# Performance work log

Hardware: AMD Instinct MI355X
Metric: run time of the kernel (lower is better)

## Reference

```python
import jax, jax.numpy as jnp
import numpy as np

B, S, D, L, H = 8, 1024, 512, 6, 8
HD = D // H


def setup_inputs() -> dict:
    key = jax.random.key(0)
    sc = D ** -0.5
    inp = {
        "xr": jax.random.normal(jax.random.fold_in(key, 0), (B, S, D), jnp.float32),
        "xi": jax.random.normal(jax.random.fold_in(key, 1), (B, S, D), jnp.float32),
    }
    wnames = ["Wq_r", "Wq_i", "Wk_r", "Wk_i", "Wv_r", "Wv_i", "Wo_r", "Wo_i",
              "W1_r", "W1_i", "W2_r", "W2_i"]
    for i, n in enumerate(wnames):
        inp[n] = jax.random.normal(jax.random.fold_in(key, 10 + i), (L, D, D), jnp.float32) * sc
    for n in ["bq_r", "bq_i", "bk_r", "bk_i", "bv_r", "bv_i", "bo_r", "bo_i",
              "b1_r", "b1_i", "b2_r", "b2_i"]:
        inp[n] = jnp.zeros((L, D), jnp.float32)
    g0 = 1.0 / np.sqrt(2.0)  # standard complex-LN affine init
    for n in ["ln1_grr", "ln1_gii", "ln2_grr", "ln2_gii"]:
        inp[n] = jnp.full((L, D), g0, jnp.float32)
    for n in ["ln1_gri", "ln1_br", "ln1_bi", "ln2_gri", "ln2_br", "ln2_bi"]:
        inp[n] = jnp.zeros((L, D), jnp.float32)
    return inp


def clin(xr, xi, Wr, Wi, br, bi):
    # ComplexLinear: (xr + i xi)(Wr + i Wi)^T + (br + i bi)
    yr = xr @ Wr.T - xi @ Wi.T + br
    yi = xr @ Wi.T + xi @ Wr.T + bi
    return yr, yi


def cln(xr, xi, grr, gri, gii, br, bi, eps=1e-5):
    # Complex LayerNorm: 2x2 covariance whitening over the feature dim + affine
    mr = xr.mean(-1, keepdims=True)
    mi = xi.mean(-1, keepdims=True)
    cr, ci = xr - mr, xi - mi
    Vrr = (cr * cr).mean(-1, keepdims=True) + eps
    Vii = (ci * ci).mean(-1, keepdims=True) + eps
    Vri = (cr * ci).mean(-1, keepdims=True)
    s = jnp.sqrt(Vrr * Vii - Vri * Vri)
    t = jnp.sqrt(Vrr + Vii + 2.0 * s)
    st = s * t
    Wrr = (Vii + s) / st
    Wii = (Vrr + s) / st
    Wri = -Vri / st
    hr = Wrr * cr + Wri * ci
    hi = Wri * cr + Wii * ci
    return grr * hr + gri * hi + br, gri * hr + gii * hi + bi


def reference(xr, xi,
              Wq_r, Wq_i, bq_r, bq_i, Wk_r, Wk_i, bk_r, bk_i,
              Wv_r, Wv_i, bv_r, bv_i, Wo_r, Wo_i, bo_r, bo_i,
              W1_r, W1_i, b1_r, b1_i, W2_r, W2_i, b2_r, b2_i,
              ln1_grr, ln1_gri, ln1_gii, ln1_br, ln1_bi,
              ln2_grr, ln2_gri, ln2_gii, ln2_br, ln2_bi):
    b, s, d = xr.shape
    nl = Wq_r.shape[0]
    h = H
    hd = d // h
    scale = hd ** -0.5
    for l in range(nl):
        rr, ri = xr, xi
        qr, qi = clin(xr, xi, Wq_r[l], Wq_i[l], bq_r[l], bq_i[l])
        kr, ki = clin(xr, xi, Wk_r[l], Wk_i[l], bk_r[l], bk_i[l])
        vr, vi = clin(xr, xi, Wv_r[l], Wv_i[l], bv_r[l], bv_i[l])
        split = lambda a: a.reshape(b, s, h, hd)
        qr, qi, kr, ki, vr, vi = map(split, (qr, qi, kr, ki, vr, vi))
        # sm_variante='real': softmax over Re(q k^H) = qr.kr + qi.ki
        logits = (jnp.einsum('bqhd,bkhd->bhqk', qr, kr)
                  + jnp.einsum('bqhd,bkhd->bhqk', qi, ki)) * scale
        A = jax.nn.softmax(logits, axis=-1)  # real-valued attention weights
        o_r = jnp.einsum('bhqk,bkhd->bqhd', A, vr).reshape(b, s, d)
        o_i = jnp.einsum('bhqk,bkhd->bqhd', A, vi).reshape(b, s, d)
        o_r, o_i = clin(o_r, o_i, Wo_r[l], Wo_i[l], bo_r[l], bo_i[l])
        xr, xi = o_r + rr, o_i + ri
        xr, xi = cln(xr, xi, ln1_grr[l], ln1_gri[l], ln1_gii[l], ln1_br[l], ln1_bi[l])
        rr, ri = xr, xi
        hr, hi = clin(xr, xi, W1_r[l], W1_i[l], b1_r[l], b1_i[l])
        hr, hi = jax.nn.relu(hr), jax.nn.relu(hi)  # CReLU; dropout = identity (eval)
        hr, hi = clin(hr, hi, W2_r[l], W2_i[l], b2_r[l], b2_i[l])
        xr, xi = hr + rr, hi + ri
        xr, xi = cln(xr, xi, ln2_grr[l], ln2_gri[l], ln2_gii[l], ln2_br[l], ln2_bi[l])
    return jnp.stack([xr, xi])  # [2, B, S, D] (real, imag)
```

## Files before the change

### kernel.cpp

```cpp
#include <hip/hip_runtime.h>
#include <cstddef>
#include <cstdint>

constexpr int NB   = 8;
constexpr int SEQ  = 1024;
constexpr int DIM  = 512;
constexpr int NL   = 6;
constexpr int NH   = 8;
constexpr int HDIM = 64;
constexpr int ROWS = NB * SEQ;
constexpr size_t BSD = (size_t)ROWS * DIM;
constexpr int KHAT = 1024;

typedef __attribute__((ext_vector_type(8))) short bfrag;
typedef __attribute__((ext_vector_type(4))) float f32x4;
typedef __attribute__((ext_vector_type(4))) unsigned short us4;

__device__ __forceinline__ void f4a(const float4 v, float* a) {
    a[0] = v.x; a[1] = v.y; a[2] = v.z; a[3] = v.w;
}
__device__ __forceinline__ float4 a4f(const float* a) {
    float4 v; v.x = a[0]; v.y = a[1]; v.z = a[2]; v.w = a[3]; return v;
}
__device__ __forceinline__ unsigned short f2bf(float f) {
    union { float f; uint32_t u; } x{f};
    return (unsigned short)((x.u + 0x7fffu + ((x.u >> 16) & 1u)) >> 16);
}
__device__ __forceinline__ float bf2f(unsigned short u) {
    union { uint32_t u; float f; } x;
    x.u = (uint32_t)u << 16;
    return x.f;
}
__device__ __forceinline__ void gload16(const unsigned short* g, void* l) {
    __builtin_amdgcn_global_load_lds(
        (const __attribute__((address_space(1))) void*)g,
        (__attribute__((address_space(3))) void*)l, 16, 0, 0);
}

struct PrepArgs {
    const float* Wr[6]; const float* Wi[6];
    const float* br[6]; const float* bi[6];
};

__global__ __launch_bounds__(256)
void prep_kernel(PrepArgs a, unsigned short* __restrict__ Ball,
                 float* __restrict__ biasall, int layer)
{
    const int lin = blockIdx.y;
    const int nh_ = blockIdx.x;
    const float* Wr = a.Wr[lin] + (size_t)layer * DIM * DIM;
    const float* Wi = a.Wi[lin] + (size_t)layer * DIM * DIM;

    bool real; int n0;
    if (lin < 3) { const int dh = nh_ & 127; real = dh < 64; n0 = (nh_ >> 7) * 64 + (dh & 63); }
    else         { real = nh_ < 512; n0 = nh_ & 511; }

    const int t = threadIdx.x;
    const int kk = (t * 4) & 511;
    const bool fh = t < 128;
    const float* src;
    float sgn = 1.f;
    if (fh) src = real ? Wr : Wi;
    else { if (real) { src = Wi; sgn = -1.f; } else src = Wr; }

    float v[4];
    f4a(*(const float4*)(src + (size_t)n0 * 512 + kk), v);
    us4 o;
    #pragma unroll
    for (int j = 0; j < 4; ++j) o[j] = f2bf(sgn * v[j]);
    *(us4*)(Ball + (size_t)lin * KHAT * KHAT + (size_t)nh_ * KHAT + t * 4) = o;
    if (t == 0)
        biasall[lin * KHAT + nh_] = real ? a.br[lin][layer * DIM + n0]
                                         : a.bi[lin][layer * DIM + n0];
}

__global__ __launch_bounds__(256)
void gemm_qkv(const unsigned short* __restrict__ Xh,
              const unsigned short* __restrict__ Ball,
              const float* __restrict__ biasall,
              unsigned short* __restrict__ Qh,
              unsigned short* __restrict__ Kh,
              unsigned short* __restrict__ Vth)
{
    __shared__ __align__(16) unsigned short Asm[128 * 32];
    __shared__ __align__(16) unsigned short Bsm[128 * 32];

    const int t = threadIdx.x, lane = t & 63, w = t >> 6;
    const int wm = w >> 1, wn = w & 1;
    const int c = lane & 15, g = lane >> 4;

    int bid = blockIdx.y * 24 + blockIdx.x;
    bid = (bid & 7) * 192 + (bid >> 3);
    const int nblk = bid % 24, mblk = bid / 24;
    const int n0g = nblk * 128;
    const int m0 = mblk * 128;
    const int lin = n0g >> 10;
    const int n0 = n0g & 1023;
    const unsigned short* Bh = Ball + (size_t)lin * KHAT * KHAT;
    const float* bias = biasall + lin * KHAT;

    f32x4 acc[4][4];
    #pragma unroll
    for (int i = 0; i < 4; ++i)
        #pragma unroll
        for (int j = 0; j < 4; ++j) acc[i][j] = (f32x4){0.f, 0.f, 0.f, 0.f};

    const int srow = (w << 4) + (lane >> 2);
    const int scol = (lane & 3) * 8;
    const unsigned short* gA0 = Xh + (size_t)(m0 + srow) * KHAT + scol;
    const unsigned short* gA1 = Xh + (size_t)(m0 + 64 + srow) * KHAT + scol;
    const unsigned short* gB0 = Bh + (size_t)(n0 + srow) * KHAT + scol;
    const unsigned short* gB1 = Bh + (size_t)(n0 + 64 + srow) * KHAT + scol;
    char* aBase = (char*)Asm + (w << 10);
    char* bBase = (char*)Bsm + (w << 10);

    for (int ks = 0; ks < 32; ++ks) {
        const int k0 = ks * 32;
        __syncthreads();
        gload16(gA0 + k0, aBase);
        gload16(gA1 + k0, aBase + 4096);
        gload16(gB0 + k0, bBase);
        gload16(gB1 + k0, bBase + 4096);
        __syncthreads();

        bfrag af[4], bf2[4];
        #pragma unroll
        for (int mi = 0; mi < 4; ++mi)
            af[mi] = *(const bfrag*)(Asm + (wm * 64 + mi * 16 + c) * 32 + g * 8);
        #pragma unroll
        for (int ni = 0; ni < 4; ++ni)
            bf2[ni] = *(const bfrag*)(Bsm + (wn * 64 + ni * 16 + c) * 32 + g * 8);
        #pragma unroll
        for (int mi = 0; mi < 4; ++mi)
            #pragma unroll
            for (int ni = 0; ni < 4; ++ni)
                acc[mi][ni] = __builtin_amdgcn_mfma_f32_16x16x32_bf16(
                    af[mi], bf2[ni], acc[mi][ni], 0, 0, 0);
    }

    const int mbase = m0 + wm * 64;
    const int nbase = n0 + wn * 64;
    unsigned short* dqk = (lin == 0) ? Qh : Kh;
    #pragma unroll
    for (int mi = 0; mi < 4; ++mi) {
        #pragma unroll
        for (int ni = 0; ni < 4; ++ni) {
            const int n = nbase + ni * 16 + c;
            const float bv = bias[n];
            float v[4];
            #pragma unroll
            for (int r = 0; r < 4; ++r) v[r] = acc[mi][ni][r] + bv;
            const int mrow = mbase + mi * 16 + g * 4;
            const int b = mrow >> 10, s = mrow & 1023;
            const int h = n >> 7, dh = n & 127;
            if (lin < 2) {
                const size_t a = ((size_t)(b * NH + h) * SEQ + s) * 128 + dh;
                #pragma unroll
                for (int r = 0; r < 4; ++r) dqk[a + (size_t)r * 128] = f2bf(v[r]);
            } else {
                const size_t a = ((size_t)(b * NH + h) * 128 + dh) * SEQ + s;
                us4 o;
                #pragma unroll
                for (int r = 0; r < 4; ++r) o[r] = f2bf(v[r]);
                *(us4*)(Vth + a) = o;
            }
        }
    }
}

template <bool RELU>
__global__ __launch_bounds__(256)
void gemm_mfma(const unsigned short* __restrict__ Xh,
               const unsigned short* __restrict__ Bh,
               const float* __restrict__ bias,
               unsigned short* __restrict__ Yh)
{
    __shared__ __align__(16) unsigned short Asm[128 * 32];
    __shared__ __align__(16) unsigned short Bsm[128 * 32];

    const int t = threadIdx.x, lane = t & 63, w = t >> 6;
    const int wm = w >> 1, wn = w & 1;
    const int c = lane & 15, g = lane >> 4;

    int bid = blockIdx.y * 8 + blockIdx.x;
    bid = (bid & 7) * 64 + (bid >> 3);
    const int n0 = (bid & 7) * 128;
    const int m0 = (bid >> 3) * 128;

    f32x4 acc[4][4];
    #pragma unroll
    for (int i = 0; i < 4; ++i)
        #pragma unroll
        for (int j = 0; j < 4; ++j) acc[i][j] = (f32x4){0.f, 0.f, 0.f, 0.f};

    const int srow = (w << 4) + (lane >> 2);
    const int scol = (lane & 3) * 8;
    const unsigned short* gA0 = Xh + (size_t)(m0 + srow) * KHAT + scol;
    const unsigned short* gA1 = Xh + (size_t)(m0 + 64 + srow) * KHAT + scol;
    const unsigned short* gB0 = Bh + (size_t)(n0 + srow) * KHAT + scol;
    const unsigned short* gB1 = Bh + (size_t)(n0 + 64 + srow) * KHAT + scol;
    char* aBase = (char*)Asm + (w << 10);
    char* bBase = (char*)Bsm + (w << 10);

    for (int ks = 0; ks < 32; ++ks) {
        const int k0 = ks * 32;
        __syncthreads();
        gload16(gA0 + k0, aBase);
        gload16(gA1 + k0, aBase + 4096);
        gload16(gB0 + k0, bBase);
        gload16(gB1 + k0, bBase + 4096);
        __syncthreads();

        bfrag af[4], bf2[4];
        #pragma unroll
        for (int mi = 0; mi < 4; ++mi)
            af[mi] = *(const bfrag*)(Asm + (wm * 64 + mi * 16 + c) * 32 + g * 8);
        #pragma unroll
        for (int ni = 0; ni < 4; ++ni)
            bf2[ni] = *(const bfrag*)(Bsm + (wn * 64 + ni * 16 + c) * 32 + g * 8);
        #pragma unroll
        for (int mi = 0; mi < 4; ++mi)
            #pragma unroll
            for (int ni = 0; ni < 4; ++ni)
                acc[mi][ni] = __builtin_amdgcn_mfma_f32_16x16x32_bf16(
                    af[mi], bf2[ni], acc[mi][ni], 0, 0, 0);
    }

    const int mbase = m0 + wm * 64;
    const int nbase = n0 + wn * 64;
    #pragma unroll
    for (int mi = 0; mi < 4; ++mi) {
        #pragma unroll
        for (int ni = 0; ni < 4; ++ni) {
            const int n = nbase + ni * 16 + c;
            const float bv = bias[n];
            const int mrow = mbase + mi * 16 + g * 4;
            #pragma unroll
            for (int r = 0; r < 4; ++r) {
                float v = acc[mi][ni][r] + bv;
                if (RELU) v = fmaxf(v, 0.f);
                Yh[(size_t)(mrow + r) * KHAT + n] = f2bf(v);
            }
        }
    }
}

__global__ __launch_bounds__(256)
void attn_mfma(const unsigned short* __restrict__ Qh,
               const unsigned short* __restrict__ Kh,
               const unsigned short* __restrict__ Vth,
               unsigned short* __restrict__ Ah)
{
    __shared__ __align__(16) char smem[41216];
    char* Ksm = smem;
    char* Vsm = smem + 16384;
    const int t    = threadIdx.x;
    const int lane = t & 63;
    const int wv   = t >> 6;
    const int c    = lane & 15;
    const int g    = lane >> 4;
    char* Pw = smem + 32768 + wv * 2048;

    int bid = blockIdx.x + 16 * blockIdx.y + 128 * blockIdx.z;
    bid = (bid & 7) * 128 + (bid >> 3);
    const int q0 = (bid & 15) * 64;
    const int bh = bid >> 4;
    const int hh = bh & 7, bb = bh >> 3;
    const size_t qkb = (size_t)bh * SEQ * 128;
    const size_t vtb = (size_t)bh * 128 * SEQ;

    constexpr float SC  = 0.125f * 1.44269504f;
    constexpr float THR = 11.0f;

    bfrag qf[4];
    {
        const unsigned short* qp = Qh + qkb + (size_t)(q0 + wv * 16 + c) * 128 + g * 8;
        #pragma unroll
        for (int ks = 0; ks < 4; ++ks) qf[ks] = *(const bfrag*)(qp + ks * 32);
    }
    bfrag vones;
    #pragma unroll
    for (int j = 0; j < 8; ++j) vones[j] = (short)0x3F80;

    f32x4 oacc[8];
    #pragma unroll
    for (int i = 0; i < 8; ++i) oacc[i] = (f32x4){0.f, 0.f, 0.f, 0.f};
    f32x4 oaccl = (f32x4){0.f, 0.f, 0.f, 0.f};
    float mrun[4];
    #pragma unroll
    for (int r = 0; r < 4; ++r) mrun[r] = -1e30f;

    const int kkey = t >> 2, kq = t & 3;
    const unsigned short* kgp = Kh + qkb + (size_t)kkey * 128 + kq * 32;
    const int vd = t >> 1, vh2 = t & 1;
    const unsigned short* vgp = Vth + vtb + (size_t)vd * SEQ + vh2 * 32;

    bfrag krg[4], vrg[4];
    #pragma unroll
    for (int j = 0; j < 4; ++j) krg[j] = *(const bfrag*)(kgp + j * 8);
    #pragma unroll
    for (int j = 0; j < 4; ++j) vrg[j] = *(const bfrag*)(vgp + j * 8);

    for (int k0 = 0; k0 < SEQ; k0 += 64) {
        __syncthreads();
        #pragma unroll
        for (int j = 0; j < 4; ++j) {
            const int boff = (kkey * 256 + (kq * 32 + j * 8) * 2) ^ ((kkey & 7) << 4);
            *(bfrag*)(Ksm + boff) = krg[j];
        }
        #pragma unroll
        for (int j = 0; j < 4; ++j) {
            const int boff = (vd * 128 + (vh2 * 32 + j * 8) * 2) ^ ((vd & 7) << 4);
            *(bfrag*)(Vsm + boff) = vrg[j];
        }
        __syncthreads();

        if (k0 + 64 < SEQ) {
            const int kn = k0 + 64;
            #pragma unroll
            for (int j = 0; j < 4; ++j) krg[j] = *(const bfrag*)(kgp + (size_t)kn * 128 + j * 8);
            #pragma unroll
            for (int j = 0; j < 4; ++j) vrg[j] = *(const bfrag*)(vgp + kn + j * 8);
        }

        f32x4 sa[4];
        #pragma unroll
        for (int nt = 0; nt < 4; ++nt) sa[nt] = (f32x4){0.f, 0.f, 0.f, 0.f};
        __builtin_amdgcn_s_setprio(1);
        #pragma unroll
        for (int nt = 0; nt < 4; ++nt) {
            const int key = nt * 16 + c;
            #pragma unroll
            for (int ks = 0; ks < 4; ++ks) {
                const int boff = (key * 256 + (ks * 32 + g * 8) * 2) ^ ((key & 7) << 4);
                const bfrag bk = *(const bfrag*)(Ksm + boff);
                sa[nt] = __builtin_amdgcn_mfma_f32_16x16x32_bf16(qf[ks], bk, sa[nt], 0, 0, 0);
            }
        }
        __builtin_amdgcn_s_setprio(0);

        float sv[4][4];
        #pragma unroll
        for (int nt = 0; nt < 4; ++nt)
            #pragma unroll
            for (int r = 0; r < 4; ++r) sv[nt][r] = sa[nt][r] * SC;

        float mloc[4];
        #pragma unroll
        for (int r = 0; r < 4; ++r)
            mloc[r] = fmaxf(fmaxf(sv[0][r], sv[1][r]), fmaxf(sv[2][r], sv[3][r]));
        bool big = false;
        #pragma unroll
        for (int r = 0; r < 4; ++r) big |= (mloc[r] > mrun[r] + THR);
        if (__any(big)) {
            float mt[4], fs[4];
            #pragma unroll
            for (int r = 0; r < 4; ++r) mt[r] = mloc[r];
            #pragma unroll
            for (int m = 1; m <= 8; m <<= 1) {
                #pragma unroll
                for (int r = 0; r < 4; ++r) mt[r] = fmaxf(mt[r], __shfl_xor(mt[r], m, 64));
            }
            #pragma unroll
            for (int r = 0; r < 4; ++r) {
                const float mn = fmaxf(mrun[r], mt[r]);
                fs[r] = exp2f(mrun[r] - mn);
                mrun[r] = mn;
            }
            const int rr = c & 3;
            float vsel = fs[0];
            vsel = (rr == 1) ? fs[1] : vsel;
            vsel = (rr == 2) ? fs[2] : vsel;
            vsel = (rr == 3) ? fs[3] : vsel;
            const float fsc = __shfl(vsel, ((c >> 2) << 4) | (c & 3), 64);
            #pragma unroll
            for (int i = 0; i < 8; ++i) {
                oacc[i][0] *= fsc; oacc[i][1] *= fsc; oacc[i][2] *= fsc; oacc[i][3] *= fsc;
            }
            oaccl[0] *= fsc; oaccl[1] *= fsc; oaccl[2] *= fsc; oaccl[3] *= fsc;
        }

        #pragma unroll
        for (int nt = 0; nt < 4; ++nt) {
            const int col2 = (nt * 16 + c) * 2;
            #pragma unroll
            for (int r = 0; r < 4; ++r) {
                const float p = exp2f(sv[nt][r] - mrun[r]);
                const int qrow = 4 * g + r;
                *(unsigned short*)(Pw + ((qrow * 128 + col2) ^ ((qrow & 7) << 4))) = f2bf(p);
            }
        }

        asm volatile("s_waitcnt lgkmcnt(0)" ::: "memory");
        __builtin_amdgcn_sched_barrier(0);

        __builtin_amdgcn_s_setprio(1);
        #pragma unroll
        for (int k2 = 0; k2 < 2; ++k2) {
            const int kb2 = (k2 * 32 + g * 8) * 2;
            const bfrag pb = *(const bfrag*)(Pw + ((c * 128 + kb2) ^ ((c & 7) << 4)));
            #pragma unroll
            for (int mtl = 0; mtl < 8; ++mtl) {
                const int d = mtl * 16 + c;
                const bfrag va = *(const bfrag*)(Vsm + ((d * 128 + kb2) ^ ((d & 7) << 4)));
                oacc[mtl] = __builtin_amdgcn_mfma_f32_16x16x32_bf16(va, pb, oacc[mtl], 0, 0, 0);
            }
            oaccl = __builtin_amdgcn_mfma_f32_16x16x32_bf16(vones, pb, oaccl, 0, 0, 0);
        }
        __builtin_amdgcn_s_setprio(0);
    }

    {
        const float ic = 1.0f / oaccl[0];
        #pragma unroll
        for (int i = 0; i < 8; ++i) {
            oacc[i][0] *= ic; oacc[i][1] *= ic; oacc[i][2] *= ic; oacc[i][3] *= ic;
        }
    }
    __syncthreads();
    float* Ox = (float*)(smem + wv * 8192);
    #pragma unroll
    for (int mtl = 0; mtl < 8; ++mtl)
        #pragma unroll
        for (int r = 0; r < 4; ++r)
            Ox[(mtl * 16 + 4 * g + r) * 16 + c] = oacc[mtl][r];
    asm volatile("s_waitcnt lgkmcnt(0)" ::: "memory");
    __builtin_amdgcn_sched_barrier(0);

    const int q = lane >> 2, qt = lane & 3;
    const int colbase = (qt >> 1) * 512 + hh * 64 + (qt & 1) * 32;
    const size_t rowm = (size_t)bb * SEQ + q0 + wv * 16 + q;
    unsigned short* dst = Ah + rowm * KHAT + colbase;
    #pragma unroll
    for (int j = 0; j < 8; ++j) {
        us4 o;
        #pragma unroll
        for (int e = 0; e < 4; ++e) o[e] = f2bf(Ox[(qt * 32 + j * 4 + e) * 16 + q]);
        *(us4*)(dst + j * 4) = o;
    }
}

__global__ __launch_bounds__(256)
void cln_kernel(const unsigned short* __restrict__ U,
                float* __restrict__ Xr, float* __restrict__ Xi,
                unsigned short* __restrict__ Xh,
                const float* __restrict__ Grr, const float* __restrict__ Gri,
                const float* __restrict__ Gii, const float* __restrict__ Bbr,
                const float* __restrict__ Bbi)
{
    const int lane = threadIdx.x & 63;
    const int row  = blockIdx.x * 4 + (threadIdx.x >> 6);
    const size_t off = (size_t)row * DIM;
    const int c0 = lane * 4;
    const int c1 = 256 + lane * 4;

    float xr[8], xi[8];
    {
        const unsigned short* up = U + (size_t)row * KHAT;
        us4 a0 = *(const us4*)(up + c0);
        us4 a1 = *(const us4*)(up + c1);
        us4 b0 = *(const us4*)(up + 512 + c0);
        us4 b1 = *(const us4*)(up + 512 + c1);
        float t0[4], t1[4];
        f4a(*(const float4*)&Xr[off + c0], t0);
        f4a(*(const float4*)&Xr[off + c1], t1);
        #pragma unroll
        for (int j = 0; j < 4; ++j) { xr[j] = bf2f(a0[j]) + t0[j]; xr[4 + j] = bf2f(a1[j]) + t1[j]; }
        f4a(*(const float4*)&Xi[off + c0], t0);
        f4a(*(const float4*)&Xi[off + c1], t1);
        #pragma unroll
        for (int j = 0; j < 4; ++j) { xi[j] = bf2f(b0[j]) + t0[j]; xi[4 + j] = bf2f(b1[j]) + t1[j]; }
    }

    float sr = 0.f, si = 0.f, srr = 0.f, sii = 0.f, sri = 0.f;
    #pragma unroll
    for (int j = 0; j < 8; ++j) {
        sr += xr[j]; si += xi[j];
        srr = fmaf(xr[j], xr[j], srr);
        sii = fmaf(xi[j], xi[j], sii);
        sri = fmaf(xr[j], xi[j], sri);
    }
    #pragma unroll
    for (int m = 32; m >= 1; m >>= 1) {
        sr  += __shfl_xor(sr,  m, 64);
        si  += __shfl_xor(si,  m, 64);
        srr += __shfl_xor(srr, m, 64);
        sii += __shfl_xor(sii, m, 64);
        sri += __shfl_xor(sri, m, 64);
    }

    const float inv_d = 1.0f / DIM;
    const float mr = sr * inv_d, mi = si * inv_d;
    const float Vrr = srr * inv_d - mr * mr + 1e-5f;
    const float Vii = sii * inv_d - mi * mi + 1e-5f;
    const float Vri = sri * inv_d - mr * mi;
    const float s  = sqrtf(Vrr * Vii - Vri * Vri);
    const float tt = sqrtf(Vrr + Vii + 2.0f * s);
    const float ist = 1.0f / (s * tt);
    const float Wrr = (Vii + s) * ist;
    const float Wii = (Vrr + s) * ist;
    const float Wri = -Vri * ist;

    #pragma unroll
    for (int half = 0; half < 2; ++half) {
        const int c = half ? c1 : c0;
        float grr[4], gri[4], gii[4], pbr[4], pbi[4];
        f4a(*(const float4*)&Grr[c], grr);
        f4a(*(const float4*)&Gri[c], gri);
        f4a(*(const float4*)&Gii[c], gii);
        f4a(*(const float4*)&Bbr[c], pbr);
        f4a(*(const float4*)&Bbi[c], pbi);
        float outr[4], outi[4];
        #pragma unroll
        for (int j = 0; j < 4; ++j) {
            const int idx = half * 4 + j;
            const float cr = xr[idx] - mr;
            const float ci = xi[idx] - mi;
            const float hr = Wrr * cr + Wri * ci;
            const float hi = Wri * cr + Wii * ci;
            outr[j] = fmaf(grr[j], hr, fmaf(gri[j], hi, pbr[j]));
            outi[j] = fmaf(gri[j], hr, fmaf(gii[j], hi, pbi[j]));
        }
        *(float4*)&Xr[off + c] = a4f(outr);
        *(float4*)&Xi[off + c] = a4f(outi);
        us4 hr_, hi_;
        #pragma unroll
        for (int j = 0; j < 4; ++j) { hr_[j] = f2bf(outr[j]); hi_[j] = f2bf(outi[j]); }
        *(us4*)(Xh + (size_t)row * KHAT + c)       = hr_;
        *(us4*)(Xh + (size_t)row * KHAT + 512 + c) = hi_;
    }
}

__global__ __launch_bounds__(256)
void init_cvt(const float* __restrict__ xr, const float* __restrict__ xi,
              float* __restrict__ outr, float* __restrict__ outi,
              unsigned short* __restrict__ Xh)
{
    const size_t i = ((size_t)blockIdx.x * 256 + threadIdx.x) * 4;
    float vr[4], vi[4];
    f4a(*(const float4*)(xr + i), vr);
    f4a(*(const float4*)(xi + i), vi);
    *(float4*)(outr + i) = a4f(vr);
    *(float4*)(outi + i) = a4f(vi);
    const size_t m = i >> 9;
    const int k = (int)(i & 511);
    us4 a, b;
    #pragma unroll
    for (int j = 0; j < 4; ++j) { a[j] = f2bf(vr[j]); b[j] = f2bf(vi[j]); }
    *(us4*)(Xh + m * KHAT + k)       = a;
    *(us4*)(Xh + m * KHAT + 512 + k) = b;
}

extern "C" void kernel_launch(void* const* d_in, const int* in_sizes, int n_in,
                              void* d_out, int out_size, void* d_ws, size_t ws_size,
                              hipStream_t stream) {
    (void)in_sizes; (void)n_in; (void)out_size; (void)ws_size;

    const float* in_xr = (const float*)d_in[0];
    const float* in_xi = (const float*)d_in[1];
    PrepArgs pa;
    pa.Wr[0] = (const float*)d_in[2];  pa.Wi[0] = (const float*)d_in[3];
    pa.Wr[1] = (const float*)d_in[4];  pa.Wi[1] = (const float*)d_in[5];
    pa.Wr[2] = (const float*)d_in[6];  pa.Wi[2] = (const float*)d_in[7];
    pa.Wr[3] = (const float*)d_in[8];  pa.Wi[3] = (const float*)d_in[9];
    pa.Wr[4] = (const float*)d_in[10]; pa.Wi[4] = (const float*)d_in[11];
    pa.Wr[5] = (const float*)d_in[12]; pa.Wi[5] = (const float*)d_in[13];
    pa.br[0] = (const float*)d_in[14]; pa.bi[0] = (const float*)d_in[15];
    pa.br[1] = (const float*)d_in[16]; pa.bi[1] = (const float*)d_in[17];
    pa.br[2] = (const float*)d_in[18]; pa.bi[2] = (const float*)d_in[19];
    pa.br[3] = (const float*)d_in[20]; pa.bi[3] = (const float*)d_in[21];
    pa.br[4] = (const float*)d_in[22]; pa.bi[4] = (const float*)d_in[23];
    pa.br[5] = (const float*)d_in[24]; pa.bi[5] = (const float*)d_in[25];
    const float* ln1_grr = (const float*)d_in[26];
    const float* ln1_gii = (const float*)d_in[27];
    const float* ln2_grr = (const float*)d_in[28];
    const float* ln2_gii = (const float*)d_in[29];
    const float* ln1_gri = (const float*)d_in[30];
    const float* ln1_br  = (const float*)d_in[31];
    const float* ln1_bi  = (const float*)d_in[32];
    const float* ln2_gri = (const float*)d_in[33];
    const float* ln2_br  = (const float*)d_in[34];
    const float* ln2_bi  = (const float*)d_in[35];

    float* outr = (float*)d_out;
    float* outi = outr + BSD;

    char* ws = (char*)d_ws;
    unsigned short* Xh  = (unsigned short*)(ws);
    unsigned short* Qh  = (unsigned short*)(ws + 16777216);
    unsigned short* Kh  = (unsigned short*)(ws + 2 * 16777216);
    unsigned short* Vth = (unsigned short*)(ws + 3 * 16777216);
    unsigned short* Ah  = (unsigned short*)(ws + 4 * 16777216);
    unsigned short* Ball = (unsigned short*)(ws + 5 * 16777216);
    float* biasall = (float*)(ws + 5 * 16777216 + 12582912);
    unsigned short* Uh = Kh;
    unsigned short* Hh = Qh;

    init_cvt<<<ROWS * DIM / 1024, 256, 0, stream>>>(in_xr, in_xi, outr, outi, Xh);

    const dim3 pgrid(KHAT, 6);
    const dim3 qgrid(24, ROWS / 128);
    const dim3 ggrid(KHAT / 128, ROWS / 128);
    const dim3 agrid(SEQ / 64, NH, NB);
    const int  lgrid = ROWS / 4;

    for (int l = 0; l < NL; ++l) {
        const size_t bo = (size_t)l * DIM;
        prep_kernel<<<pgrid, 256, 0, stream>>>(pa, Ball, biasall, l);

        unsigned short* Bo = Ball + (size_t)3 * KHAT * KHAT;
        unsigned short* B1 = Ball + (size_t)4 * KHAT * KHAT;
        unsigned short* B2 = Ball + (size_t)5 * KHAT * KHAT;

        gemm_qkv<<<qgrid, 256, 0, stream>>>(Xh, Ball, biasall, Qh, Kh, Vth);
        attn_mfma<<<agrid, 256, 0, stream>>>(Qh, Kh, Vth, Ah);
        gemm_mfma<false><<<ggrid, 256, 0, stream>>>(Ah, Bo, biasall + 3 * KHAT, Uh);
        cln_kernel<<<lgrid, 256, 0, stream>>>(Uh, outr, outi, Xh,
                                              ln1_grr + bo, ln1_gri + bo, ln1_gii + bo,
                                              ln1_br + bo, ln1_bi + bo);
        gemm_mfma<true><<<ggrid, 256, 0, stream>>>(Xh, B1, biasall + 4 * KHAT, Hh);
        gemm_mfma<false><<<ggrid, 256, 0, stream>>>(Hh, B2, biasall + 5 * KHAT, Uh);
        cln_kernel<<<lgrid, 256, 0, stream>>>(Uh, outr, outi, Xh,
                                              ln2_grr + bo, ln2_gri + bo, ln2_gii + bo,
                                              ln2_br + bo, ln2_bi + bo);
    }
}
```

Measured before the change: 1.516 ms.

## Keep attention probabilities in registers via transposed QK MFMA and permuted V layout

Swaps the MFMA operand order for QK^T so each lane holds scores for a single query column, then packs probabilities straight into bf16 B-fragments for the PV MFMA. This drops the per-wave LDS round trip for P and its wait. To make register fragments line up with the key order, the V^T layout written by the projection kernel is permuted in 32-key chunks. The row sum is now kept as a scalar running value with shuffles instead of an extra ones-vector MFMA. LDS use falls from 41 KB to 32 KB, which may allow more resident blocks. The cost is extra exp/add work and cross-lane shuffles in the softmax, plus a tight coupling between the V layout and the fragment packing.

```diff
diff --git a/kernel.cpp b/kernel.cpp
--- a/kernel.cpp
+++ b/kernel.cpp
@@ -30,6 +30,11 @@
     union { uint32_t u; float f; } x;
     x.u = (uint32_t)u << 16;
     return x.f;
+}
+__device__ __forceinline__ uint32_t cvtpk(float lo, float hi) {
+    uint32_t r;
+    asm("v_cvt_pk_bf16_f32 %0, %1, %2" : "=v"(r) : "v"(lo), "v"(hi));
+    return r;
 }
 __device__ __forceinline__ void gload16(const unsigned short* g, void* l) {
     __builtin_amdgcn_global_load_lds(
@@ -158,7 +163,9 @@
                 #pragma unroll
                 for (int r = 0; r < 4; ++r) dqk[a + (size_t)r * 128] = f2bf(v[r]);
             } else {
-                const size_t a = ((size_t)(b * NH + h) * 128 + dh) * SEQ + s;
+                const int ck = (s & 31) >> 2;
+                const int sp = (s & ~31) | ((((ck & 3) << 1) | (ck >> 2)) << 2);
+                const size_t a = ((size_t)(b * NH + h) * 128 + dh) * SEQ + sp;
                 us4 o;
                 #pragma unroll
                 for (int r = 0; r < 4; ++r) o[r] = f2bf(v[r]);
@@ -251,7 +258,7 @@
                const unsigned short* __restrict__ Vth,
                unsigned short* __restrict__ Ah)
 {
-    __shared__ __align__(16) char smem[41216];
+    __shared__ __align__(16) char smem[32768];
     char* Ksm = smem;
     char* Vsm = smem + 16384;
     const int t    = threadIdx.x;
@@ -259,7 +266,6 @@
     const int wv   = t >> 6;
     const int c    = lane & 15;
     const int g    = lane >> 4;
-    char* Pw = smem + 32768 + wv * 2048;
 
     int bid = blockIdx.x + 16 * blockIdx.y + 128 * blockIdx.z;
     bid = (bid & 7) * 128 + (bid >> 3);
@@ -278,17 +284,11 @@
         #pragma unroll
         for (int ks = 0; ks < 4; ++ks) qf[ks] = *(const bfrag*)(qp + ks * 32);
     }
-    bfrag vones;
-    #pragma unroll
-    for (int j = 0; j < 8; ++j) vones[j] = (short)0x3F80;
 
     f32x4 oacc[8];
     #pragma unroll
     for (int i = 0; i < 8; ++i) oacc[i] = (f32x4){0.f, 0.f, 0.f, 0.f};
-    f32x4 oaccl = (f32x4){0.f, 0.f, 0.f, 0.f};
-    float mrun[4];
-    #pragma unroll
-    for (int r = 0; r < 4; ++r) mrun[r] = -1e30f;
+    float mrun = -1e30f, lrun = 0.f;
 
     const int kkey = t >> 2, kq = t & 3;
     const unsigned short* kgp = Kh + qkb + (size_t)kkey * 128 + kq * 32;
@@ -334,7 +334,7 @@
             for (int ks = 0; ks < 4; ++ks) {
                 const int boff = (key * 256 + (ks * 32 + g * 8) * 2) ^ ((key & 7) << 4);
                 const bfrag bk = *(const bfrag*)(Ksm + boff);
-                sa[nt] = __builtin_amdgcn_mfma_f32_16x16x32_bf16(qf[ks], bk, sa[nt], 0, 0, 0);
+                sa[nt] = __builtin_amdgcn_mfma_f32_16x16x32_bf16(bk, qf[ks], sa[nt], 0, 0, 0);
             }
         }
         __builtin_amdgcn_s_setprio(0);
@@ -345,73 +345,66 @@
             #pragma unroll
             for (int r = 0; r < 4; ++r) sv[nt][r] = sa[nt][r] * SC;
 
-        float mloc[4];
-        #pragma unroll
-        for (int r = 0; r < 4; ++r)
-            mloc[r] = fmaxf(fmaxf(sv[0][r], sv[1][r]), fmaxf(sv[2][r], sv[3][r]));
-        bool big = false;
-        #pragma unroll
-        for (int r = 0; r < 4; ++r) big |= (mloc[r] > mrun[r] + THR);
-        if (__any(big)) {
-            float mt[4], fs[4];
-            #pragma unroll
-            for (int r = 0; r < 4; ++r) mt[r] = mloc[r];
-            #pragma unroll
-            for (int m = 1; m <= 8; m <<= 1) {
-                #pragma unroll
-                for (int r = 0; r < 4; ++r) mt[r] = fmaxf(mt[r], __shfl_xor(mt[r], m, 64));
+        float mloc = sv[0][0];
+        #pragma unroll
+        for (int nt = 0; nt < 4; ++nt)
+            #pragma unroll
+            for (int r = 0; r < 4; ++r) mloc = fmaxf(mloc, sv[nt][r]);
+        if (__any(mloc > mrun + THR)) {
+            float mt = mloc;
+            mt = fmaxf(mt, __shfl_xor(mt, 16, 64));
+            mt = fmaxf(mt, __shfl_xor(mt, 32, 64));
+            const float mn = fmaxf(mrun, mt);
+            const float fs = exp2f(mrun - mn);
+            mrun = mn;
+            lrun *= fs;
+            #pragma unroll
+            for (int i = 0; i < 8; ++i) {
+                oacc[i][0] *= fs; oacc[i][1] *= fs; oacc[i][2] *= fs; oacc[i][3] *= fs;
             }
+        }
+
+        float p[4][4];
+        float psum = 0.f;
+        #pragma unroll
+        for (int nt = 0; nt < 4; ++nt)
             #pragma unroll
             for (int r = 0; r < 4; ++r) {
-                const float mn = fmaxf(mrun[r], mt[r]);
-                fs[r] = exp2f(mrun[r] - mn);
-                mrun[r] = mn;
+                p[nt][r] = exp2f(sv[nt][r] - mrun);
+                psum += p[nt][r];
             }
-            const int rr = c & 3;
-            float vsel = fs[0];
-            vsel = (rr == 1) ? fs[1] : vsel;
-            vsel = (rr == 2) ? fs[2] : vsel;
-            vsel = (rr == 3) ? fs[3] : vsel;
-            const float fsc = __shfl(vsel, ((c >> 2) << 4) | (c & 3), 64);
-            #pragma unroll
-            for (int i = 0; i < 8; ++i) {
-                oacc[i][0] *= fsc; oacc[i][1] *= fsc; oacc[i][2] *= fsc; oacc[i][3] *= fsc;
-            }
-            oaccl[0] *= fsc; oaccl[1] *= fsc; oaccl[2] *= fsc; oaccl[3] *= fsc;
-        }
-
+        psum += __shfl_xor(psum, 16, 64);
+        psum += __shfl_xor(psum, 32, 64);
+        lrun += psum;
+
+        uint32_t pk0[4], pk1[4];
         #pragma unroll
         for (int nt = 0; nt < 4; ++nt) {
-            const int col2 = (nt * 16 + c) * 2;
-            #pragma unroll
-            for (int r = 0; r < 4; ++r) {
-                const float p = exp2f(sv[nt][r] - mrun[r]);
-                const int qrow = 4 * g + r;
-                *(unsigned short*)(Pw + ((qrow * 128 + col2) ^ ((qrow & 7) << 4))) = f2bf(p);
-            }
-        }
-
-        asm volatile("s_waitcnt lgkmcnt(0)" ::: "memory");
-        __builtin_amdgcn_sched_barrier(0);
+            pk0[nt] = cvtpk(p[nt][0], p[nt][1]);
+            pk1[nt] = cvtpk(p[nt][2], p[nt][3]);
+        }
 
         __builtin_amdgcn_s_setprio(1);
         #pragma unroll
         for (int k2 = 0; k2 < 2; ++k2) {
+            union { uint32_t u[4]; bfrag f; } pb;
+            pb.u[0] = pk0[2 * k2];
+            pb.u[1] = pk1[2 * k2];
+            pb.u[2] = pk0[2 * k2 + 1];
+            pb.u[3] = pk1[2 * k2 + 1];
             const int kb2 = (k2 * 32 + g * 8) * 2;
-            const bfrag pb = *(const bfrag*)(Pw + ((c * 128 + kb2) ^ ((c & 7) << 4)));
             #pragma unroll
             for (int mtl = 0; mtl < 8; ++mtl) {
                 const int d = mtl * 16 + c;
                 const bfrag va = *(const bfrag*)(Vsm + ((d * 128 + kb2) ^ ((d & 7) << 4)));
-                oacc[mtl] = __builtin_amdgcn_mfma_f32_16x16x32_bf16(va, pb, oacc[mtl], 0, 0, 0);
+                oacc[mtl] = __builtin_amdgcn_mfma_f32_16x16x32_bf16(va, pb.f, oacc[mtl], 0, 0, 0);
             }
-            oaccl = __builtin_amdgcn_mfma_f32_16x16x32_bf16(vones, pb, oaccl, 0, 0, 0);
         }
         __builtin_amdgcn_s_setprio(0);
     }
 
     {
-        const float ic = 1.0f / oaccl[0];
+        const float ic = 1.0f / lrun;
         #pragma unroll
         for (int i = 0; i < 8; ++i) {
             oacc[i][0] *= ic; oacc[i][1] *= ic; oacc[i][2] *= ic; oacc[i][3] *= ic;
```

Measured after the change: 1.522 ms. About the same (+0.4%).
